# Optimization experiments

Hardware: AMD Instinct MI355X
Metric: run time of the kernel (lower is better)

Reference implementation:

```python
import jax, jax.numpy as jnp
import numpy as np

NUM_HEADS = 8
NUM_GROUPS = 32
EPS = 1e-5


def setup_inputs() -> dict:
    key = jax.random.key(0)
    ks = jax.random.split(key, 7)
    B, C, H, W = 8, 512, 32, 32
    x = jax.random.normal(ks[0], (B, C, H, W), dtype=jnp.float32)
    # GroupNorm affine params
    gn_w = jnp.ones((C,), dtype=jnp.float32)
    gn_b = jnp.zeros((C,), dtype=jnp.float32)
    # 1x1 conv == linear over channel dim; store squeezed weights (out, in)
    qkv_w = jax.random.normal(ks[1], (3 * C, C), dtype=jnp.float32) * (1.0 / np.sqrt(C))
    qkv_b = jnp.zeros((3 * C,), dtype=jnp.float32)
    proj_w = jax.random.normal(ks[2], (C, C), dtype=jnp.float32) * (1.0 / np.sqrt(C))
    proj_b = jnp.zeros((C,), dtype=jnp.float32)
    return {"x": x, "gn_w": gn_w, "gn_b": gn_b, "qkv_w": qkv_w,
            "qkv_b": qkv_b, "proj_w": proj_w, "proj_b": proj_b}


def reference(x, gn_w, gn_b, qkv_w, qkv_b, proj_w, proj_b):
    B, C, H, W = x.shape
    G = NUM_GROUPS
    hd = C // NUM_HEADS
    scale = hd ** -0.5
    # GroupNorm: normalize over (C//G, H, W) per group
    xg = x.reshape(B, G, C // G, H, W)
    mean = xg.mean(axis=(2, 3, 4), keepdims=True)
    var = xg.var(axis=(2, 3, 4), keepdims=True)
    xn = ((xg - mean) * jax.lax.rsqrt(var + EPS)).reshape(B, C, H, W)
    xn = xn * gn_w[None, :, None, None] + gn_b[None, :, None, None]
    # QKV 1x1 conv
    qkv = jnp.einsum('bchw,oc->bohw', xn, qkv_w) + qkv_b[None, :, None, None]
    # (B, 3, heads, head_dim, HW) -> (3, B, heads, HW, head_dim)
    qkv = qkv.reshape(B, 3, NUM_HEADS, hd, H * W).transpose(1, 0, 2, 4, 3)
    q, k, v = qkv[0], qkv[1], qkv[2]
    attn = jax.nn.softmax(jnp.einsum('bhqd,bhkd->bhqk', q, k) * scale, axis=-1)
    out = jnp.einsum('bhqk,bhkd->bhqd', attn, v)  # (B, heads, HW, hd)
    out = out.transpose(0, 1, 3, 2).reshape(B, C, H, W)
    out = jnp.einsum('bchw,oc->bohw', out, proj_w) + proj_b[None, :, None, None]
    return out + x
```

## Files before the change

### kernel.cpp

```cpp
#include <hip/hip_runtime.h>
#include <hip/hip_bf16.h>
#include <math.h>

typedef __bf16 bf16_t;
typedef __bf16 bf16x8 __attribute__((ext_vector_type(8)));
typedef __bf16 bf16x4 __attribute__((ext_vector_type(4)));
typedef float  f32x4  __attribute__((ext_vector_type(4)));
typedef short  short4v __attribute__((ext_vector_type(4)));

#define NB    8
#define NC    512
#define NHW   1024
#define NHEAD 8
#define NHD   64
#define NG    32
#define NCG   16
#define NO3   1536
#define KVB   64
#define NKT   16

__device__ __forceinline__ void lds_load16(bf16_t* lds, const bf16_t* g) {
  __builtin_amdgcn_global_load_lds(
      (__attribute__((address_space(1))) unsigned int*)(g),
      (__attribute__((address_space(3))) unsigned int*)(void*)(lds),
      16, 0, 0);
}

__device__ __forceinline__ f32x4 mfma16(bf16x4 a, bf16x4 b, f32x4 c) {
#if __has_builtin(__builtin_amdgcn_mfma_f32_16x16x16bf16_1k)
  return __builtin_amdgcn_mfma_f32_16x16x16bf16_1k(
      __builtin_bit_cast(short4v, a), __builtin_bit_cast(short4v, b), c, 0, 0, 0);
#else
  f32x4 d;
  asm("v_mfma_f32_16x16x16_bf16 %0, %1, %2, %3"
      : "=v"(d) : "v"(a), "v"(b), "v"(c));
  return d;
#endif
}

__device__ __forceinline__ float fexp2(float x) {
#if __has_builtin(__builtin_amdgcn_exp2f)
  return __builtin_amdgcn_exp2f(x);
#else
  return exp2f(x);
#endif
}

__global__ __launch_bounds__(256)
void gnw_kernel(const float* __restrict__ x, const float* __restrict__ gw,
                const float* __restrict__ gb, bf16_t* __restrict__ xn,
                const float* __restrict__ qw, const float* __restrict__ pw,
                bf16_t* __restrict__ qwb, bf16_t* __restrict__ pwb)
{
  const int bid = blockIdx.x;
  const int tid = threadIdx.x;

  if (bid >= NB * NG) {
    const int gid = (bid - NB * NG) * 256 + tid;
    const int n1 = NO3 * NC / 4;
    float4 v; bf16x4 o;
    if (gid < n1) {
      v = ((const float4*)qw)[gid];
      o[0] = (bf16_t)v.x; o[1] = (bf16_t)v.y; o[2] = (bf16_t)v.z; o[3] = (bf16_t)v.w;
      ((bf16x4*)qwb)[gid] = o;
    } else {
      int g2 = gid - n1;
      v = ((const float4*)pw)[g2];
      o[0] = (bf16_t)v.x; o[1] = (bf16_t)v.y; o[2] = (bf16_t)v.z; o[3] = (bf16_t)v.w;
      ((bf16x4*)pwb)[g2] = o;
    }
    return;
  }

  const int b = bid >> 5, g = bid & 31;
  const float* xp = x + ((size_t)b * NC + g * NCG) * NHW;
  const int wave = tid >> 6, lane = tid & 63;

  float4 v[16];
  const float4* xp4 = (const float4*)xp;
  float s1 = 0.f, s2 = 0.f;
  #pragma unroll
  for (int c = 0; c < 16; ++c) {
    v[c] = xp4[c * 256 + tid];
    s1 += v[c].x + v[c].y + v[c].z + v[c].w;
    s2 += v[c].x * v[c].x + v[c].y * v[c].y + v[c].z * v[c].z + v[c].w * v[c].w;
  }
  for (int off = 32; off > 0; off >>= 1) {
    s1 += __shfl_down(s1, off);
    s2 += __shfl_down(s2, off);
  }
  __shared__ float red[16];
  if (lane == 0) { red[wave] = s1; red[8 + wave] = s2; }
  __syncthreads();
  float tot1 = red[0] + red[1] + red[2] + red[3];
  float tot2 = red[8] + red[9] + red[10] + red[11];
  const float mean = tot1 * (1.0f / 16384.0f);
  const float var  = tot2 * (1.0f / 16384.0f) - mean * mean;
  const float rstd = rsqrtf(var + 1e-5f);

  float gam[NCG], bet[NCG];
  #pragma unroll
  for (int c = 0; c < NCG; ++c) {
    gam[c] = gw[g * NCG + c] * rstd;
    bet[c] = gb[g * NCG + c] - mean * gam[c];
  }
  bf16_t* op = xn + (size_t)b * NHW * NC + g * NCG;
  #pragma unroll
  for (int jj = 0; jj < 4; ++jj) {
    int s = 4 * tid + jj;
    __align__(16) bf16_t vals[NCG];
    #pragma unroll
    for (int c = 0; c < NCG; ++c) {
      float xv = (jj == 0) ? v[c].x : (jj == 1) ? v[c].y : (jj == 2) ? v[c].z : v[c].w;
      vals[c] = (bf16_t)(xv * gam[c] + bet[c]);
    }
    *(bf16x8*)(op + (size_t)s * NC)     = *(const bf16x8*)&vals[0];
    *(bf16x8*)(op + (size_t)s * NC + 8) = *(const bf16x8*)&vals[8];
  }
}

__global__ __launch_bounds__(256, 2)
void qkv_gemm(const bf16_t* __restrict__ xn, const bf16_t* __restrict__ w,
              const float* __restrict__ bias,
              bf16_t* __restrict__ qbuf, bf16_t* __restrict__ kbuf, bf16_t* __restrict__ vbuf)
{
  __shared__ __align__(16) char smem[34816];
  const int tid = threadIdx.x;
  const int wave = tid >> 6, lane = tid & 63;
  const int quad = lane >> 4, l16 = lane & 15;
  const int wm = wave >> 1, wn = wave & 1;
  const int bx = blockIdx.x, by = blockIdx.y, b = blockIdx.z;

  const bf16_t* Ap = xn + ((size_t)b * NHW + by * 128) * NC;
  const bf16_t* Bp = w + (size_t)bx * 128 * NC;

  auto stage = [&](int k0, int bufi) {
    bf16_t* sA = (bf16_t*)(smem + bufi * 16384);
    bf16_t* sB = (bf16_t*)(smem + bufi * 16384 + 8192);
    #pragma unroll
    for (int j = 0; j < 2; ++j) {
      int c = wave * 64 + j * 256 + lane;
      int row = c >> 2, ko = (c & 3) * 8;
      lds_load16(sA + (size_t)(wave * 64 + j * 256) * 8, Ap + (size_t)row * 512 + k0 + ko);
      lds_load16(sB + (size_t)(wave * 64 + j * 256) * 8, Bp + (size_t)row * 512 + k0 + ko);
    }
  };

  f32x4 acc[4][4] = {};
  stage(0, 0);
  __syncthreads();
  for (int t = 0; t < 16; ++t) {
    const int cur = t & 1;
    if (t < 15) stage((t + 1) * 32, cur ^ 1);
    const bf16_t* sA = (const bf16_t*)(smem + cur * 16384);
    const bf16_t* sB = sA + 4096;
    bf16x8 af[4], bfr[4];
    #pragma unroll
    for (int mi = 0; mi < 4; ++mi)
      af[mi] = *(const bf16x8*)(sA + (wm * 64 + mi * 16 + l16) * 32 + quad * 8);
    #pragma unroll
    for (int ni = 0; ni < 4; ++ni)
      bfr[ni] = *(const bf16x8*)(sB + (wn * 64 + ni * 16 + l16) * 32 + quad * 8);
    #pragma unroll
    for (int mi = 0; mi < 4; ++mi)
      #pragma unroll
      for (int ni = 0; ni < 4; ++ni)
        acc[mi][ni] = __builtin_amdgcn_mfma_f32_16x16x32_bf16(af[mi], bfr[ni], acc[mi][ni], 0, 0, 0);
    __syncthreads();
  }

  const int obase = bx * 128 + wn * 64;
  const int sbase = by * 128 + wm * 64;
  float bv[4];
  #pragma unroll
  for (int ni = 0; ni < 4; ++ni) bv[ni] = bias[obase + ni * 16 + l16];

  if (bx < 8) {
    const bool isq = (bx < 4);
    bf16_t* basep = isq ? qbuf : kbuf;
    const float scale = isq ? 0.18033688f : 1.0f;
    #pragma unroll
    for (int ni = 0; ni < 4; ++ni) {
      int o = obase + ni * 16 + l16;
      int hh = (o >> 6) & 7, dd = o & 63;
      bf16_t* dst = basep + ((size_t)(b * NHEAD + hh) * NHW) * NHD + dd;
      #pragma unroll
      for (int mi = 0; mi < 4; ++mi)
        #pragma unroll
        for (int r = 0; r < 4; ++r) {
          int s = sbase + mi * 16 + quad * 4 + r;
          dst[(size_t)s * NHD] = (bf16_t)((acc[mi][ni][r] + bv[ni]) * scale);
        }
    }
  } else {
    bf16_t* sC = (bf16_t*)smem;
    __syncthreads();
    #pragma unroll
    for (int ni = 0; ni < 4; ++ni)
      #pragma unroll
      for (int mi = 0; mi < 4; ++mi)
        #pragma unroll
        for (int r = 0; r < 4; ++r)
          sC[(wn * 64 + ni * 16 + l16) * 136 + wm * 64 + mi * 16 + quad * 4 + r] =
              (bf16_t)(acc[mi][ni][r] + bv[ni]);
    __syncthreads();
    int o_local = tid >> 1, shalf = (tid & 1) << 6;
    int ov = (bx - 8) * 128 + o_local;
    int hh = ov >> 6, dd = ov & 63;
    bf16_t* dst = vbuf + ((size_t)(b * NHEAD + hh) * NHD + dd) * NHW + by * 128 + shalf;
    #pragma unroll
    for (int jj = 0; jj < 8; ++jj)
      *(bf16x8*)(dst + jj * 8) = *(const bf16x8*)&sC[o_local * 136 + shalf + jj * 8];
  }
}

__global__ __launch_bounds__(256, 2)
void attn_kernel(const bf16_t* __restrict__ qbuf, const bf16_t* __restrict__ kbuf,
                 const bf16_t* __restrict__ vbuf, bf16_t* __restrict__ obuf)
{
  __shared__ __align__(16) char smem[32768];
  f32x4* mO = (f32x4*)smem;
  float* mM = (float*)(smem + 16384);
  float* mL = (float*)(smem + 17408);

  const int tid = threadIdx.x;
  const int wave = tid >> 6, lane = tid & 63;
  const int quad = lane >> 4, l16 = lane & 15;
  const int wl = wave & 1;
  const int wg = wave >> 1;
  const int idx = blockIdx.x;
  const int qt = idx >> 6, h = (idx >> 3) & 7, b = idx & 7;
  const size_t bh = (size_t)b * NHEAD + h;
  const bf16_t* qp = qbuf + (bh * NHW + qt * 64 + wl * 32) * NHD;
  const char* kp = (const char*)(kbuf + bh * NHW * NHD);
  const char* vp = (const char*)(vbuf + bh * NHD * NHW);

  const int r8 = lane >> 3;
  const int swc = (((lane & 7) << 4)) ^ (r8 << 4);

  bf16x8 qf[2][2];
  #pragma unroll
  for (int stile = 0; stile < 2; ++stile)
    #pragma unroll
    for (int kc = 0; kc < 2; ++kc)
      qf[stile][kc] = *(const bf16x8*)(qp + (size_t)(stile * 16 + l16) * NHD + kc * 32 + quad * 8);

  float m_i[2] = {-1e30f, -1e30f};
  float ll[2] = {0.f, 0.f};
  f32x4 oacc[4][2] = {};

  #pragma unroll
  for (int j = 0; j < 2; ++j) {
    int i = wave * 2 + j;
    const char* kg = kp + ((size_t)(i * 8 + r8) * NHD) * 2 + swc;
    lds_load16((bf16_t*)(smem + i * 1024), (const bf16_t*)kg);
    const char* vg = vp + ((size_t)(i * 8 + r8) * NHW) * 2 + swc;
    lds_load16((bf16_t*)(smem + 8192 + i * 1024), (const bf16_t*)vg);
  }
  __syncthreads();

  const int swr = (l16 & 7) << 4;

  for (int kt = 0; kt < NKT; ++kt) {
    const int cur = kt & 1;
    const char* Kb = smem + cur * 16384;
    const char* Vb = Kb + 8192;
    if (kt < NKT - 1) {
      char* Kn = smem + (cur ^ 1) * 16384;
      #pragma unroll
      for (int j = 0; j < 2; ++j) {
        int i = wave * 2 + j;
        const char* kg = kp + ((size_t)((kt + 1) * KVB + i * 8 + r8) * NHD) * 2 + swc;
        lds_load16((bf16_t*)(Kn + i * 1024), (const bf16_t*)kg);
        const char* vg = vp + ((size_t)(i * 8 + r8) * NHW + (kt + 1) * KVB) * 2 + swc;
        lds_load16((bf16_t*)(Kn + 8192 + i * 1024), (const bf16_t*)vg);
      }
    }

    f32x4 st[2][2];
    __builtin_amdgcn_s_setprio(1);
    #pragma unroll
    for (int mt = 0; mt < 2; ++mt) {
      const int mtg = wg * 2 + mt;
      const char* krow = Kb + (mtg * 16 + l16) * 128;
      bf16x8 ka0 = *(const bf16x8*)(krow + ((quad * 16) ^ swr));
      bf16x8 ka1 = *(const bf16x8*)(krow + ((64 + quad * 16) ^ swr));
      #pragma unroll
      for (int stile = 0; stile < 2; ++stile) {
        f32x4 z = {};
        z = __builtin_amdgcn_mfma_f32_16x16x32_bf16(ka0, qf[stile][0], z, 0, 0, 0);
        z = __builtin_amdgcn_mfma_f32_16x16x32_bf16(ka1, qf[stile][1], z, 0, 0, 0);
        st[stile][mt] = z;
      }
    }
    __builtin_amdgcn_s_setprio(0);

    #pragma unroll
    for (int stile = 0; stile < 2; ++stile) {
      float mx = st[stile][0][0];
      #pragma unroll
      for (int mt = 0; mt < 2; ++mt)
        #pragma unroll
        for (int r = 0; r < 4; ++r) mx = fmaxf(mx, st[stile][mt][r]);
      if (!__all(mx <= m_i[stile])) {
        mx = fmaxf(mx, __shfl_xor(mx, 16));
        mx = fmaxf(mx, __shfl_xor(mx, 32));
        float mnew = fmaxf(m_i[stile], mx);
        float alpha = fexp2(m_i[stile] - mnew);
        m_i[stile] = mnew;
        ll[stile] *= alpha;
        #pragma unroll
        for (int mi = 0; mi < 4; ++mi)
          #pragma unroll
          for (int r = 0; r < 4; ++r) oacc[mi][stile][r] *= alpha;
      }
      float rs = 0.f;
      #pragma unroll
      for (int mt = 0; mt < 2; ++mt)
        #pragma unroll
        for (int r = 0; r < 4; ++r) {
          float p = fexp2(st[stile][mt][r] - m_i[stile]);
          rs += p;
          st[stile][mt][r] = p;
        }
      ll[stile] += rs;
    }

    __builtin_amdgcn_s_setprio(1);
    #pragma unroll
    for (int mt = 0; mt < 2; ++mt) {
      const int mtg = wg * 2 + mt;
      bf16x4 pb[2];
      #pragma unroll
      for (int stile = 0; stile < 2; ++stile) {
        pb[stile][0] = (bf16_t)st[stile][mt][0];
        pb[stile][1] = (bf16_t)st[stile][mt][1];
        pb[stile][2] = (bf16_t)st[stile][mt][2];
        pb[stile][3] = (bf16_t)st[stile][mt][3];
      }
      #pragma unroll
      for (int mi = 0; mi < 4; ++mi) {
        const char* vrow = Vb + (mi * 16 + l16) * 128;
        bf16x4 va = *(const bf16x4*)(vrow + ((mtg * 32 + quad * 8) ^ swr));
        oacc[mi][0] = mfma16(va, pb[0], oacc[mi][0]);
        oacc[mi][1] = mfma16(va, pb[1], oacc[mi][1]);
      }
    }
    __builtin_amdgcn_s_setprio(0);
    __syncthreads();
  }

  float l_i[2];
  #pragma unroll
  for (int stile = 0; stile < 2; ++stile) {
    float rs = ll[stile];
    rs += __shfl_xor(rs, 16);
    rs += __shfl_xor(rs, 32);
    l_i[stile] = rs;
  }

  if (wg == 1) {
    #pragma unroll
    for (int stile = 0; stile < 2; ++stile) {
      mM[(wl * 2 + stile) * 64 + lane] = m_i[stile];
      mL[(wl * 2 + stile) * 64 + lane] = l_i[stile];
      #pragma unroll
      for (int mi = 0; mi < 4; ++mi)
        mO[((wl * 2 + stile) * 4 + mi) * 64 + lane] = oacc[mi][stile];
    }
  }
  __syncthreads();
  if (wg == 0) {
    #pragma unroll
    for (int stile = 0; stile < 2; ++stile) {
      float mB = mM[(wl * 2 + stile) * 64 + lane];
      float lB = mL[(wl * 2 + stile) * 64 + lane];
      float mS = fmaxf(m_i[stile], mB);
      float aA = fexp2(m_i[stile] - mS);
      float aB = fexp2(mB - mS);
      float inv = 1.0f / (l_i[stile] * aA + lB * aB);
      int s = qt * 64 + wl * 32 + stile * 16 + l16;
      bf16_t* orow = obuf + ((size_t)b * NHW + s) * NC + h * NHD;
      #pragma unroll
      for (int mi = 0; mi < 4; ++mi) {
        f32x4 oB = mO[((wl * 2 + stile) * 4 + mi) * 64 + lane];
        __align__(8) bf16_t o4[4];
        #pragma unroll
        for (int r = 0; r < 4; ++r)
          o4[r] = (bf16_t)((oacc[mi][stile][r] * aA + oB[r] * aB) * inv);
        *(bf16x4*)(orow + mi * 16 + quad * 4) = *(const bf16x4*)o4;
      }
    }
  }
}

__global__ __launch_bounds__(256, 2)
void proj_gemm(const bf16_t* __restrict__ ob, const bf16_t* __restrict__ w,
               const float* __restrict__ bias, const float* __restrict__ x,
               float* __restrict__ out)
{
  __shared__ __align__(16) char smem[24576];
  const int tid = threadIdx.x;
  const int wave = tid >> 6, lane = tid & 63;
  const int quad = lane >> 4, l16 = lane & 15;
  const int wm = wave & 1, wn = wave >> 1;
  const int bx = blockIdx.x, by = blockIdx.y, b = blockIdx.z;

  const bf16_t* Ap = w + (size_t)by * 64 * NC;
  const bf16_t* Bp = ob + ((size_t)b * NHW + bx * 128) * NC;

  auto stage = [&](int k0, int bufi) {
    bf16_t* sA = (bf16_t*)(smem + bufi * 12288);
    bf16_t* sB = (bf16_t*)(smem + bufi * 12288 + 4096);
    {
      int c = wave * 64 + lane;
      int row = c >> 2, ko = (c & 3) * 8;
      lds_load16(sA + (size_t)(wave * 64) * 8, Ap + (size_t)row * 512 + k0 + ko);
    }
    #pragma unroll
    for (int j = 0; j < 2; ++j) {
      int c = wave * 64 + j * 256 + lane;
      int row = c >> 2, ko = (c & 3) * 8;
      lds_load16(sB + (size_t)(wave * 64 + j * 256) * 8, Bp + (size_t)row * 512 + k0 + ko);
    }
  };

  f32x4 acc[2][4] = {};
  stage(0, 0);
  __syncthreads();
  for (int t = 0; t < 16; ++t) {
    const int cur = t & 1;
    if (t < 15) stage((t + 1) * 32, cur ^ 1);
    const bf16_t* sA = (const bf16_t*)(smem + cur * 12288);
    const bf16_t* sB = sA + 2048;
    bf16x8 af[2], bfr[4];
    #pragma unroll
    for (int mi = 0; mi < 2; ++mi)
      af[mi] = *(const bf16x8*)(sA + (wm * 32 + mi * 16 + l16) * 32 + quad * 8);
    #pragma unroll
    for (int ni = 0; ni < 4; ++ni)
      bfr[ni] = *(const bf16x8*)(sB + (wn * 64 + ni * 16 + l16) * 32 + quad * 8);
    #pragma unroll
    for (int mi = 0; mi < 2; ++mi)
      #pragma unroll
      for (int ni = 0; ni < 4; ++ni)
        acc[mi][ni] = __builtin_amdgcn_mfma_f32_16x16x32_bf16(af[mi], bfr[ni], acc[mi][ni], 0, 0, 0);
    __syncthreads();
  }

  const int cobase = by * 64 + wm * 32;
  const int sbase  = bx * 128 + wn * 64;
  #pragma unroll
  for (int mi = 0; mi < 2; ++mi)
    #pragma unroll
    for (int r = 0; r < 4; ++r) {
      int co = cobase + mi * 16 + quad * 4 + r;
      float pb = bias[co];
      const float* xrow = x + ((size_t)b * NC + co) * NHW;
      float* orow = out + ((size_t)b * NC + co) * NHW;
      #pragma unroll
      for (int ni = 0; ni < 4; ++ni) {
        int s = sbase + ni * 16 + l16;
        orow[s] = acc[mi][ni][r] + pb + xrow[s];
      }
    }
}

extern "C" void kernel_launch(void* const* d_in, const int* in_sizes, int n_in,
                              void* d_out, int out_size, void* d_ws, size_t ws_size,
                              hipStream_t stream)
{
  const float* x      = (const float*)d_in[0];
  const float* gn_w   = (const float*)d_in[1];
  const float* gn_b   = (const float*)d_in[2];
  const float* qkv_w  = (const float*)d_in[3];
  const float* qkv_b  = (const float*)d_in[4];
  const float* proj_w = (const float*)d_in[5];
  const float* proj_b = (const float*)d_in[6];
  float* out = (float*)d_out;

  char* ws = (char*)d_ws;
  bf16_t* xn   = (bf16_t*)(ws);
  bf16_t* qwb  = (bf16_t*)(ws + 8388608);
  bf16_t* pwb  = (bf16_t*)(ws + 9961472);
  bf16_t* qbuf = (bf16_t*)(ws + 10485760);
  bf16_t* kbuf = (bf16_t*)(ws + 18874368);
  bf16_t* vbuf = (bf16_t*)(ws + 27262976);
  bf16_t* obuf = xn;

  gnw_kernel<<<dim3(NB * NG + 1024), dim3(256), 0, stream>>>(
      x, gn_w, gn_b, xn, qkv_w, proj_w, qwb, pwb);
  qkv_gemm<<<dim3(12, 8, NB), dim3(256), 0, stream>>>(xn, qwb, qkv_b, qbuf, kbuf, vbuf);
  attn_kernel<<<dim3(1024), dim3(256), 0, stream>>>(qbuf, kbuf, vbuf, obuf);
  proj_gemm<<<dim3(8, 8, NB), dim3(256), 0, stream>>>(obuf, pwb, proj_b, x, out);
}
```

Measured before the change: 152.4 us.

## Load K/V fragments directly from global memory instead of LDS double buffering

Removes the double-buffered LDS staging of K and V tiles (global_load_lds with swizzle) and has each wave read its MFMA operands straight from global memory. This drops the per-iteration __syncthreads and s_setprio hints and shrinks shared memory, which could raise occupancy. In exchange, K/V tiles are fetched redundantly by waves, so the loop now leans on L1/L2 hits, and there is no explicit prefetch to overlap load latency with compute.

```diff
diff --git a/kernel.cpp b/kernel.cpp
--- a/kernel.cpp
+++ b/kernel.cpp
@@ -218,10 +218,10 @@
 void attn_kernel(const bf16_t* __restrict__ qbuf, const bf16_t* __restrict__ kbuf,
                  const bf16_t* __restrict__ vbuf, bf16_t* __restrict__ obuf)
 {
-  __shared__ __align__(16) char smem[32768];
+  __shared__ __align__(16) char smem[18432];
   f32x4* mO = (f32x4*)smem;
   float* mM = (float*)(smem + 16384);
-  float* mL = (float*)(smem + 17408);
+  float* mL = mM + 256;
 
   const int tid = threadIdx.x;
   const int wave = tid >> 6, lane = tid & 63;
@@ -232,11 +232,8 @@
   const int qt = idx >> 6, h = (idx >> 3) & 7, b = idx & 7;
   const size_t bh = (size_t)b * NHEAD + h;
   const bf16_t* qp = qbuf + (bh * NHW + qt * 64 + wl * 32) * NHD;
-  const char* kp = (const char*)(kbuf + bh * NHW * NHD);
-  const char* vp = (const char*)(vbuf + bh * NHD * NHW);
-
-  const int r8 = lane >> 3;
-  const int swc = (((lane & 7) << 4)) ^ (r8 << 4);
+  const bf16_t* kp = kbuf + bh * NHW * NHD;
+  const bf16_t* vp = vbuf + bh * NHD * NHW;
 
   bf16x8 qf[2][2];
   #pragma unroll
@@ -249,42 +246,16 @@
   float ll[2] = {0.f, 0.f};
   f32x4 oacc[4][2] = {};
 
-  #pragma unroll
-  for (int j = 0; j < 2; ++j) {
-    int i = wave * 2 + j;
-    const char* kg = kp + ((size_t)(i * 8 + r8) * NHD) * 2 + swc;
-    lds_load16((bf16_t*)(smem + i * 1024), (const bf16_t*)kg);
-    const char* vg = vp + ((size_t)(i * 8 + r8) * NHW) * 2 + swc;
-    lds_load16((bf16_t*)(smem + 8192 + i * 1024), (const bf16_t*)vg);
-  }
-  __syncthreads();
-
-  const int swr = (l16 & 7) << 4;
+  const bf16_t* krow0 = kp + (size_t)(wg * 32 + l16) * NHD;
+  const bf16_t* vrow0 = vp + (size_t)l16 * NHW + wg * 32 + quad * 4;
 
   for (int kt = 0; kt < NKT; ++kt) {
-    const int cur = kt & 1;
-    const char* Kb = smem + cur * 16384;
-    const char* Vb = Kb + 8192;
-    if (kt < NKT - 1) {
-      char* Kn = smem + (cur ^ 1) * 16384;
-      #pragma unroll
-      for (int j = 0; j < 2; ++j) {
-        int i = wave * 2 + j;
-        const char* kg = kp + ((size_t)((kt + 1) * KVB + i * 8 + r8) * NHD) * 2 + swc;
-        lds_load16((bf16_t*)(Kn + i * 1024), (const bf16_t*)kg);
-        const char* vg = vp + ((size_t)(i * 8 + r8) * NHW + (kt + 1) * KVB) * 2 + swc;
-        lds_load16((bf16_t*)(Kn + 8192 + i * 1024), (const bf16_t*)vg);
-      }
-    }
-
     f32x4 st[2][2];
-    __builtin_amdgcn_s_setprio(1);
     #pragma unroll
     for (int mt = 0; mt < 2; ++mt) {
-      const int mtg = wg * 2 + mt;
-      const char* krow = Kb + (mtg * 16 + l16) * 128;
-      bf16x8 ka0 = *(const bf16x8*)(krow + ((quad * 16) ^ swr));
-      bf16x8 ka1 = *(const bf16x8*)(krow + ((64 + quad * 16) ^ swr));
+      const bf16_t* krow = krow0 + (size_t)(kt * KVB + mt * 16) * NHD;
+      bf16x8 ka0 = *(const bf16x8*)(krow + quad * 8);
+      bf16x8 ka1 = *(const bf16x8*)(krow + 32 + quad * 8);
       #pragma unroll
       for (int stile = 0; stile < 2; ++stile) {
         f32x4 z = {};
@@ -293,7 +264,6 @@
         st[stile][mt] = z;
       }
     }
-    __builtin_amdgcn_s_setprio(0);
 
     #pragma unroll
     for (int stile = 0; stile < 2; ++stile) {
@@ -326,10 +296,8 @@
       ll[stile] += rs;
     }
 
-    __builtin_amdgcn_s_setprio(1);
     #pragma unroll
     for (int mt = 0; mt < 2; ++mt) {
-      const int mtg = wg * 2 + mt;
       bf16x4 pb[2];
       #pragma unroll
       for (int stile = 0; stile < 2; ++stile) {
@@ -340,14 +308,11 @@
       }
       #pragma unroll
       for (int mi = 0; mi < 4; ++mi) {
-        const char* vrow = Vb + (mi * 16 + l16) * 128;
-        bf16x4 va = *(const bf16x4*)(vrow + ((mtg * 32 + quad * 8) ^ swr));
+        bf16x4 va = *(const bf16x4*)(vrow0 + (size_t)mi * 16 * NHW + kt * KVB + mt * 16);
         oacc[mi][0] = mfma16(va, pb[0], oacc[mi][0]);
         oacc[mi][1] = mfma16(va, pb[1], oacc[mi][1]);
       }
     }
-    __builtin_amdgcn_s_setprio(0);
-    __syncthreads();
   }
 
   float l_i[2];
```

After: 207.3 us. 36.0% more time.
